# Kernel optimization log

Hardware: AMD Instinct MI355X
Metric: run time of the kernel (lower is better)

Reference implementation:

```python
import jax, jax.numpy as jnp
import numpy as np

ATT_DIM, HID_DIM, EMB_DIM = 512, 1024, 1024
SEQ_LEN, BATCH = 2048, 32


def setup_inputs() -> dict:
    key = jax.random.key(0)
    k1, k2, k3, k4, k5, k6, k7 = jax.random.split(key, 7)
    s_h = 1.0 / np.sqrt(HID_DIM)
    s_e = 1.0 / np.sqrt(EMB_DIM)
    return {
        "hid": jax.random.normal(k1, (BATCH, HID_DIM), dtype=jnp.float32),
        "emb": jax.random.normal(k2, (SEQ_LEN, BATCH, EMB_DIM), dtype=jnp.float32),
        "W_hid": jax.random.uniform(k3, (HID_DIM, ATT_DIM), jnp.float32, -s_h, s_h),
        "b_hid": jax.random.uniform(k4, (ATT_DIM,), jnp.float32, -s_h, s_h),
        "W_emb": jax.random.uniform(k5, (EMB_DIM, ATT_DIM), jnp.float32, -s_e, s_e),
        "b_emb": jax.random.uniform(k6, (ATT_DIM,), jnp.float32, -s_e, s_e),
        "att_v": jax.random.normal(k7, (ATT_DIM,), dtype=jnp.float32),
    }


def reference(hid, emb, W_hid, b_hid, W_emb, b_emb, att_v):
    # hid:  (B, H)   emb: (S, B, E)
    hid_att = hid @ W_hid + b_hid                       # (B, A)
    emb_att = jnp.einsum('sbe,ea->sba', emb, W_emb) + b_emb  # (S, B, A)
    att = jnp.tanh(emb_att + hid_att[None, :, :])       # (S, B, A)
    scores = jnp.einsum('sba,a->bs', att, att_v)        # (B, S)
    weights = jax.nn.softmax(scores, axis=-1)           # (B, S)
    context = jnp.einsum('bs,sbe->be', weights, emb)    # (B, E)
    return context, weights
```

## Files before the change

kernel.cpp:

```cpp
#include <hip/hip_runtime.h>
#include <hip/hip_bf16.h>

#define S_LEN 2048
#define NB    32
#define EMB   1024
#define ATT   512
#define HID   1024

typedef float f32x4  __attribute__((ext_vector_type(4)));
typedef short s16x4  __attribute__((ext_vector_type(4)));
typedef short s16x8  __attribute__((ext_vector_type(8)));

static __device__ __forceinline__ short f2bf(float f) {
    return __builtin_bit_cast(short, __float2bfloat16(f));
}
static __device__ __forceinline__ float bf2f(unsigned short u) {
    unsigned int x = ((unsigned int)u) << 16;
    return __builtin_bit_cast(float, x);
}
static __device__ __forceinline__ float tanh_fast(float x) {
    float e = __expf(2.0f * x);
    return 1.0f - 2.0f / (e + 1.0f);
}

#define GLOAD_LDS16(gp, lp)                                                   \
    __builtin_amdgcn_global_load_lds(                                         \
        (const __attribute__((address_space(1))) void*)(gp),                  \
        (__attribute__((address_space(3))) void*)(uintptr_t)(lp), 16, 0, 0)

__global__ void k_pre(const float* __restrict__ emb,
                      const float* __restrict__ hid,
                      const float* __restrict__ W_hid,
                      const float* __restrict__ b_hid,
                      const float* __restrict__ W_emb,
                      const float* __restrict__ b_emb,
                      unsigned short* __restrict__ embB,
                      float* __restrict__ hid_comb,
                      unsigned short* __restrict__ WT) {
    __shared__ __align__(16) char lds[32768];
    int blk = blockIdx.x, tid = threadIdx.x;
    if (blk >= 576) {
        int cb = blk - 576;
        size_t base = (size_t)cb * 32768;
#pragma unroll
        for (int j = 0; j < 4; ++j)
            GLOAD_LDS16(emb + base + (j * 256 + tid) * 4, lds + (j * 256 + tid) * 16);
        for (int i = 0; i < 8; ++i) {
            int cn = (i + 1) & 7, bn = (i + 1) & 1;
#pragma unroll
            for (int j = 0; j < 4; ++j)
                GLOAD_LDS16(emb + base + cn * 4096 + (j * 256 + tid) * 4,
                            lds + bn * 16384 + (j * 256 + tid) * 16);
            asm volatile("s_waitcnt vmcnt(4)\n\ts_barrier" ::: "memory");
            const char* buf = lds + (i & 1) * 16384;
#pragma unroll
            for (int k = 0; k < 4; ++k) {
                f32x4 x = *(const f32x4*)(buf + k * 4096 + tid * 16);
                s16x4 r;
                r[0] = f2bf(x[0]); r[1] = f2bf(x[1]);
                r[2] = f2bf(x[2]); r[3] = f2bf(x[3]);
                *(s16x4*)(embB + base + i * 4096 + k * 1024 + tid * 4) = r;
            }
            asm volatile("s_waitcnt lgkmcnt(0)\n\ts_barrier" ::: "memory");
        }
    } else if (blk < 64) {
        f32x4 (*red)[64] = (f32x4(*)[64])lds;
        int b    = blk >> 1;
        int a4   = (tid & 63) * 4 + (blk & 1) * 256;
        int ks   = tid >> 6;
        int k0   = ks * 256;
        const float* hr = hid + b * HID + k0;
        const float* wp = W_hid + (size_t)k0 * ATT + a4;
        f32x4 acc = {0.f, 0.f, 0.f, 0.f};
        for (int kb = 0; kb < 256; kb += 8) {
            f32x4 x[8];
#pragma unroll
            for (int u = 0; u < 8; ++u)
                x[u] = *(const f32x4*)(wp + (size_t)(kb + u) * ATT);
            float h[8];
#pragma unroll
            for (int u = 0; u < 8; ++u) h[u] = hr[kb + u];
#pragma unroll
            for (int u = 0; u < 8; ++u) acc += h[u] * x[u];
        }
        red[ks][tid & 63] = acc;
        __syncthreads();
        if (ks == 0) {
            int al = tid & 63;
            f32x4 s = acc + red[1][al] + red[2][al] + red[3][al];
            f32x4 bh = *(const f32x4*)(b_hid + a4);
            f32x4 be = *(const f32x4*)(b_emb + a4);
            *(f32x4*)(hid_comb + b * ATT + a4) = s + bh + be;
        }
    } else {
        float (*tile)[33] = (float(*)[33])lds;
        int b2 = blk - 64;
        int k0 = (b2 & 31) * 32, a0 = (b2 >> 5) * 32;
        int tx = tid & 31, ty = tid >> 5;
#pragma unroll
        for (int i = 0; i < 32; i += 8)
            tile[ty + i][tx] = W_emb[(size_t)(k0 + ty + i) * ATT + a0 + tx];
        __syncthreads();
#pragma unroll
        for (int i = 0; i < 32; i += 8)
            WT[(size_t)(a0 + ty + i) * HID + k0 + tx] =
                (unsigned short)f2bf(tile[tx][ty + i]);
    }
}

__global__ __launch_bounds__(512) void k_gemm_scores(
        const unsigned short* __restrict__ embB,
        const unsigned short* __restrict__ WT,
        const float* __restrict__ hid_comb,
        const float* __restrict__ att_v,
        float* __restrict__ part) {
    __shared__ __align__(16) unsigned short ldsbuf[65536];
    char* L = (char*)ldsbuf;

    int bid = blockIdx.x;
    int t2  = (bid & 7) * 64 + (bid >> 3);
    int mt  = t2 >> 1, nt = t2 & 1;
    int m0  = mt * 256, n0 = nt * 256;

    int tid  = threadIdx.x;
    int lane = tid & 63, wv = tid >> 6;
    int wm = wv >> 2, wn = wv & 3;
    int row_l = lane & 15, kg = lane >> 4;

    int row0 = tid >> 3, pos0 = tid & 7;
    int dst0 = tid * 16, dst1 = tid * 16 + 8192;
    const unsigned short* aG[2][2];
    const unsigned short* bG[2][2];
#pragma unroll
    for (int h = 0; h < 2; ++h) {
        aG[h][0] = embB + (size_t)(m0 + h * 128 + row0) * EMB + ((pos0 ^ (row0 & 7)) * 8);
        aG[h][1] = embB + (size_t)(m0 + h * 128 + row0 + 64) * EMB + ((pos0 ^ (row0 & 7)) * 8);
        bG[h][0] = WT   + (size_t)(n0 + h * 128 + row0) * HID + ((pos0 ^ (row0 & 7)) * 8);
        bG[h][1] = WT   + (size_t)(n0 + h * 128 + row0 + 64) * HID + ((pos0 ^ (row0 & 7)) * 8);
    }

    int aoff[8], boff[4], cx[2];
#pragma unroll
    for (int mf = 0; mf < 8; ++mf)
        aoff[mf] = wm * 16384 + (mf * 16 + row_l) * 128;
#pragma unroll
    for (int nf = 0; nf < 4; ++nf)
        boff[nf] = 65536 + (wn >> 1) * 16384 + (((wn & 1) * 64 + nf * 16 + row_l)) * 128;
#pragma unroll
    for (int ks = 0; ks < 2; ++ks)
        cx[ks] = ((ks * 4 + kg) ^ (row_l & 7)) * 16;

    f32x4 acc[8][4] = {};

#define STAGE_A(H, KT, BUF)                                                    \
    GLOAD_LDS16(aG[H][0] + (KT), L + (BUF) * 32768 + (H) * 16384 + dst0);      \
    GLOAD_LDS16(aG[H][1] + (KT), L + (BUF) * 32768 + (H) * 16384 + dst1);
#define STAGE_B(H, KT, BUF)                                                    \
    GLOAD_LDS16(bG[H][0] + (KT), L + 65536 + (BUF) * 32768 + (H) * 16384 + dst0); \
    GLOAD_LDS16(bG[H][1] + (KT), L + 65536 + (BUF) * 32768 + (H) * 16384 + dst1);

#define QUAD(MB, NBASE, AF, BF)                                                \
    _Pragma("unroll")                                                          \
    for (int ml = 0; ml < 4; ++ml)                                             \
        _Pragma("unroll")                                                      \
        for (int nl = 0; nl < 2; ++nl)                                         \
            _Pragma("unroll")                                                  \
            for (int ks = 0; ks < 2; ++ks)                                     \
                acc[(MB) + ml][(NBASE) + nl] =                                 \
                    __builtin_amdgcn_mfma_f32_16x16x32_bf16(                   \
                        AF[ml][ks], BF[nl][ks], acc[(MB) + ml][(NBASE) + nl],  \
                        0, 0, 0);

    STAGE_A(0, 0, 0) STAGE_A(1, 0, 0) STAGE_B(0, 0, 0) STAGE_B(1, 0, 0)

    for (int t = 0; t < 16; ++t) {
        int bt = t & 1, bn = bt ^ 1;
        int btA = bt * 32768;
        int ktn = ((t + 1) & 15) * 64;
        s16x8 af[4][2], af2[4][2], bfA[2][2], bfB[2][2];

        STAGE_A(0, ktn, bn)
        asm volatile("s_waitcnt vmcnt(2)" ::: "memory");
        asm volatile("s_barrier" ::: "memory");
#pragma unroll
        for (int ml = 0; ml < 4; ++ml)
#pragma unroll
            for (int ks = 0; ks < 2; ++ks)
                af[ml][ks] = *(const s16x8*)(L + btA + aoff[ml] + cx[ks]);
#pragma unroll
        for (int nl = 0; nl < 2; ++nl)
#pragma unroll
            for (int ks = 0; ks < 2; ++ks)
                bfA[nl][ks] = *(const s16x8*)(L + btA + boff[nl] + cx[ks]);
        asm volatile("s_waitcnt lgkmcnt(0)" ::: "memory");
        __builtin_amdgcn_sched_barrier(0);
        __builtin_amdgcn_s_setprio(1);
        QUAD(0, 0, af, bfA)
        __builtin_amdgcn_s_setprio(0);
        asm volatile("s_barrier" ::: "memory");

        STAGE_A(1, ktn, bn)
#pragma unroll
        for (int nl = 0; nl < 2; ++nl)
#pragma unroll
            for (int ks = 0; ks < 2; ++ks)
                bfB[nl][ks] = *(const s16x8*)(L + btA + boff[2 + nl] + cx[ks]);
        asm volatile("s_waitcnt lgkmcnt(0)" ::: "memory");
        __builtin_amdgcn_sched_barrier(0);
        __builtin_amdgcn_s_setprio(1);
        QUAD(0, 2, af, bfB)
        __builtin_amdgcn_s_setprio(0);
        asm volatile("s_barrier" ::: "memory");

        STAGE_B(0, ktn, bn)
#pragma unroll
        for (int ml = 0; ml < 4; ++ml)
#pragma unroll
            for (int ks = 0; ks < 2; ++ks)
                af2[ml][ks] = *(const s16x8*)(L + btA + aoff[4 + ml] + cx[ks]);
        asm volatile("s_waitcnt lgkmcnt(0)" ::: "memory");
        __builtin_amdgcn_sched_barrier(0);
        __builtin_amdgcn_s_setprio(1);
        QUAD(4, 2, af2, bfB)
        __builtin_amdgcn_s_setprio(0);
        asm volatile("s_barrier" ::: "memory");

        STAGE_B(1, ktn, bn)
        __builtin_amdgcn_s_setprio(1);
        QUAD(4, 0, af2, bfA)
        __builtin_amdgcn_s_setprio(0);
        asm volatile("s_barrier" ::: "memory");
    }
#undef STAGE_A
#undef STAGE_B
#undef QUAD

    float vvv[4];
#pragma unroll
    for (int nf = 0; nf < 4; ++nf)
        vvv[nf] = att_v[n0 + wn * 64 + nf * 16 + row_l];

    int slice = nt * 4 + wn;
#pragma unroll
    for (int mf = 0; mf < 8; ++mf) {
#pragma unroll
        for (int j = 0; j < 4; ++j) {
            int m = m0 + wm * 128 + mf * 16 + kg * 4 + j;
            int b = m & 31;
            int s = m >> 5;
            const float* ad = hid_comb + b * ATT + n0 + wn * 64;
            float sum = 0.f;
#pragma unroll
            for (int nf = 0; nf < 4; ++nf) {
                float xv = acc[mf][nf][j] + ad[nf * 16 + row_l];
                sum += tanh_fast(xv) * vvv[nf];
            }
#pragma unroll
            for (int d = 1; d < 16; d <<= 1)
                sum += __shfl_xor(sum, d, 64);
            if (row_l == 0)
                part[slice * (NB * S_LEN) + b * S_LEN + s] = sum;
        }
    }
}

__global__ void k_ctx1s(const unsigned short* __restrict__ embB,
                        const float* __restrict__ part,
                        float* __restrict__ weights,
                        float* __restrict__ cpart) {
    int sc = blockIdx.x, b = blockIdx.y, t = threadIdx.x;
    __shared__ float sm[4], ss[4], wl[128];

    float v[8];
    float mx = -1e30f;
#pragma unroll
    for (int i = 0; i < 8; ++i) {
        int s = i * 256 + t;
        float x = 0.f;
#pragma unroll
        for (int p = 0; p < 8; ++p)
            x += part[p * (NB * S_LEN) + b * S_LEN + s];
        v[i] = x;
        mx = fmaxf(mx, x);
    }
#pragma unroll
    for (int d = 1; d < 64; d <<= 1) mx = fmaxf(mx, __shfl_xor(mx, d, 64));
    if ((t & 63) == 0) sm[t >> 6] = mx;
    __syncthreads();
    mx = fmaxf(fmaxf(sm[0], sm[1]), fmaxf(sm[2], sm[3]));
    float sum = 0.f;
#pragma unroll
    for (int i = 0; i < 8; ++i) {
        v[i] = __expf(v[i] - mx);
        sum += v[i];
    }
#pragma unroll
    for (int d = 1; d < 64; d <<= 1) sum += __shfl_xor(sum, d, 64);
    if ((t & 63) == 0) ss[t >> 6] = sum;
    __syncthreads();
    sum = ss[0] + ss[1] + ss[2] + ss[3];
    float inv = 1.0f / sum;

    if ((t >> 7) == (sc & 1)) wl[t & 127] = v[sc >> 1] * inv;
    if (sc == 0) {
#pragma unroll
        for (int i = 0; i < 8; ++i)
            weights[b * S_LEN + i * 256 + t] = v[i] * inv;
    }
    __syncthreads();

    int par = t >> 7;
    int e0 = (t & 127) * 8;
    float acc[8] = {};
    for (int i = 0; i < 128; i += 2) {
        int s = sc * 128 + i + par;
        float w = wl[i + par];
        s16x8 x = *(const s16x8*)(embB + (((size_t)(s * NB + b)) << 10) + e0);
#pragma unroll
        for (int u = 0; u < 8; ++u)
            acc[u] += w * bf2f((unsigned short)x[u]);
    }
    float* dst = cpart + ((size_t)(sc * 2 + par) * NB + b) * EMB + e0;
    f32x4 lo = {acc[0], acc[1], acc[2], acc[3]};
    f32x4 hi = {acc[4], acc[5], acc[6], acc[7]};
    *(f32x4*)(dst)     = lo;
    *(f32x4*)(dst + 4) = hi;
}

__global__ void k_ctx2(const float* __restrict__ cpart, float* __restrict__ ctx) {
    int i = blockIdx.x * 256 + threadIdx.x;
    float s = 0.f;
#pragma unroll
    for (int p = 0; p < 32; ++p) s += cpart[(size_t)p * (NB * EMB) + i];
    ctx[i] = s;
}

extern "C" void kernel_launch(void* const* d_in, const int* in_sizes, int n_in,
                              void* d_out, int out_size, void* d_ws, size_t ws_size,
                              hipStream_t stream) {
    const float* hid   = (const float*)d_in[0];
    const float* emb   = (const float*)d_in[1];
    const float* W_hid = (const float*)d_in[2];
    const float* b_hid = (const float*)d_in[3];
    const float* W_emb = (const float*)d_in[4];
    const float* b_emb = (const float*)d_in[5];
    const float* att_v = (const float*)d_in[6];

    float* out     = (float*)d_out;
    float* ctx     = out;
    float* weights = out + NB * EMB;

    char* ws = (char*)d_ws;
    float*          part     = (float*)(ws);
    float*          hid_comb = (float*)(ws + 2097152);
    unsigned short* WT       = (unsigned short*)(ws + 2162688);
    unsigned short* embB     = (unsigned short*)(ws + 3211264);
    float*          cpart    = (float*)(ws + 137428992);

    k_pre<<<2624, 256, 0, stream>>>(emb, hid, W_hid, b_hid, W_emb, b_emb,
                                    embB, hid_comb, WT);
    k_gemm_scores<<<512, 512, 0, stream>>>(embB, WT, hid_comb, att_v, part);
    k_ctx1s<<<dim3(16, NB), 256, 0, stream>>>(embB, part, weights, cpart);
    k_ctx2<<<128, 256, 0, stream>>>(cpart, ctx);
}
```

Baseline: 220.8 us.

## Fuse fp32-to-bf16 conversion of emb into GEMM A-tile loading

```diff
diff --git a/kernel.cpp b/kernel.cpp
--- a/kernel.cpp
+++ b/kernel.cpp
@@ -14,10 +14,6 @@
 static __device__ __forceinline__ short f2bf(float f) {
     return __builtin_bit_cast(short, __float2bfloat16(f));
 }
-static __device__ __forceinline__ float bf2f(unsigned short u) {
-    unsigned int x = ((unsigned int)u) << 16;
-    return __builtin_bit_cast(float, x);
-}
 static __device__ __forceinline__ float tanh_fast(float x) {
     float e = __expf(2.0f * x);
     return 1.0f - 2.0f / (e + 1.0f);
@@ -28,42 +24,18 @@
         (const __attribute__((address_space(1))) void*)(gp),                  \
         (__attribute__((address_space(3))) void*)(uintptr_t)(lp), 16, 0, 0)
 
-__global__ void k_pre(const float* __restrict__ emb,
-                      const float* __restrict__ hid,
-                      const float* __restrict__ W_hid,
-                      const float* __restrict__ b_hid,
-                      const float* __restrict__ W_emb,
-                      const float* __restrict__ b_emb,
-                      unsigned short* __restrict__ embB,
-                      float* __restrict__ hid_comb,
-                      unsigned short* __restrict__ WT) {
-    __shared__ __align__(16) char lds[32768];
+#define ORDER_FENCE() asm volatile("" ::: "memory")
+
+__global__ void k_hw(const float* __restrict__ hid,
+                     const float* __restrict__ W_hid,
+                     const float* __restrict__ b_hid,
+                     const float* __restrict__ W_emb,
+                     const float* __restrict__ b_emb,
+                     float* __restrict__ hid_comb,
+                     unsigned short* __restrict__ WT) {
+    __shared__ __align__(16) char lds[8192];
     int blk = blockIdx.x, tid = threadIdx.x;
-    if (blk >= 576) {
-        int cb = blk - 576;
-        size_t base = (size_t)cb * 32768;
-#pragma unroll
-        for (int j = 0; j < 4; ++j)
-            GLOAD_LDS16(emb + base + (j * 256 + tid) * 4, lds + (j * 256 + tid) * 16);
-        for (int i = 0; i < 8; ++i) {
-            int cn = (i + 1) & 7, bn = (i + 1) & 1;
-#pragma unroll
-            for (int j = 0; j < 4; ++j)
-                GLOAD_LDS16(emb + base + cn * 4096 + (j * 256 + tid) * 4,
-                            lds + bn * 16384 + (j * 256 + tid) * 16);
-            asm volatile("s_waitcnt vmcnt(4)\n\ts_barrier" ::: "memory");
-            const char* buf = lds + (i & 1) * 16384;
-#pragma unroll
-            for (int k = 0; k < 4; ++k) {
-                f32x4 x = *(const f32x4*)(buf + k * 4096 + tid * 16);
-                s16x4 r;
-                r[0] = f2bf(x[0]); r[1] = f2bf(x[1]);
-                r[2] = f2bf(x[2]); r[3] = f2bf(x[3]);
-                *(s16x4*)(embB + base + i * 4096 + k * 1024 + tid * 4) = r;
-            }
-            asm volatile("s_waitcnt lgkmcnt(0)\n\ts_barrier" ::: "memory");
-        }
-    } else if (blk < 64) {
+    if (blk < 64) {
         f32x4 (*red)[64] = (f32x4(*)[64])lds;
         int b    = blk >> 1;
         int a4   = (tid & 63) * 4 + (blk & 1) * 256;
@@ -109,7 +81,7 @@
 }
 
 __global__ __launch_bounds__(512) void k_gemm_scores(
-        const unsigned short* __restrict__ embB,
+        const float* __restrict__ emb,
         const unsigned short* __restrict__ WT,
         const float* __restrict__ hid_comb,
         const float* __restrict__ att_v,
@@ -127,16 +99,20 @@
     int wm = wv >> 2, wn = wv & 3;
     int row_l = lane & 15, kg = lane >> 4;
 
+    int ar = tid >> 3, ap = tid & 7;
+    const float* aG0 = emb + (size_t)(m0 + ar) * EMB + ap * 8;
+    const float* aG1 = emb + (size_t)(m0 + 128 + ar) * EMB + ap * 8;
+    int axor = (ap ^ (ar & 7)) * 16;
+    int da0 = ar * 128 + axor;
+    int da1 = (ar + 64) * 128 + axor;
+
     int row0 = tid >> 3, pos0 = tid & 7;
     int dst0 = tid * 16, dst1 = tid * 16 + 8192;
-    const unsigned short* aG[2][2];
     const unsigned short* bG[2][2];
 #pragma unroll
     for (int h = 0; h < 2; ++h) {
-        aG[h][0] = embB + (size_t)(m0 + h * 128 + row0) * EMB + ((pos0 ^ (row0 & 7)) * 8);
-        aG[h][1] = embB + (size_t)(m0 + h * 128 + row0 + 64) * EMB + ((pos0 ^ (row0 & 7)) * 8);
-        bG[h][0] = WT   + (size_t)(n0 + h * 128 + row0) * HID + ((pos0 ^ (row0 & 7)) * 8);
-        bG[h][1] = WT   + (size_t)(n0 + h * 128 + row0 + 64) * HID + ((pos0 ^ (row0 & 7)) * 8);
+        bG[h][0] = WT + (size_t)(n0 + h * 128 + row0) * HID + ((pos0 ^ (row0 & 7)) * 8);
+        bG[h][1] = WT + (size_t)(n0 + h * 128 + row0 + 64) * HID + ((pos0 ^ (row0 & 7)) * 8);
     }
 
     int aoff[8], boff[4], cx[2];
@@ -151,10 +127,29 @@
         cx[ks] = ((ks * 4 + kg) ^ (row_l & 7)) * 16;
 
     f32x4 acc[8][4] = {};
-
-#define STAGE_A(H, KT, BUF)                                                    \
-    GLOAD_LDS16(aG[H][0] + (KT), L + (BUF) * 32768 + (H) * 16384 + dst0);      \
-    GLOAD_LDS16(aG[H][1] + (KT), L + (BUF) * 32768 + (H) * 16384 + dst1);
+    f32x4 Rh0[4], Rh1[4];
+
+#define LOAD_RH(RH, SRC, KT)                                                   \
+    RH[0] = *(const f32x4*)((SRC) + (KT));                                     \
+    RH[1] = *(const f32x4*)((SRC) + (KT) + 4);                                 \
+    RH[2] = *(const f32x4*)((SRC) + (KT) + 64 * EMB);                          \
+    RH[3] = *(const f32x4*)((SRC) + (KT) + 64 * EMB + 4);
+
+#define CVT_WRITE_A(RH, OFF)                                                   \
+    {                                                                          \
+        s16x8 v0, v1;                                                          \
+        v0[0] = f2bf(RH[0][0]); v0[1] = f2bf(RH[0][1]);                        \
+        v0[2] = f2bf(RH[0][2]); v0[3] = f2bf(RH[0][3]);                        \
+        v0[4] = f2bf(RH[1][0]); v0[5] = f2bf(RH[1][1]);                        \
+        v0[6] = f2bf(RH[1][2]); v0[7] = f2bf(RH[1][3]);                        \
+        v1[0] = f2bf(RH[2][0]); v1[1] = f2bf(RH[2][1]);                        \
+        v1[2] = f2bf(RH[2][2]); v1[3] = f2bf(RH[2][3]);                        \
+        v1[4] = f2bf(RH[3][0]); v1[5] = f2bf(RH[3][1]);                        \
+        v1[6] = f2bf(RH[3][2]); v1[7] = f2bf(RH[3][3]);                        \
+        *(s16x8*)(L + (OFF) + da0) = v0;                                       \
+        *(s16x8*)(L + (OFF) + da1) = v1;                                       \
+    }
+
 #define STAGE_B(H, KT, BUF)                                                    \
     GLOAD_LDS16(bG[H][0] + (KT), L + 65536 + (BUF) * 32768 + (H) * 16384 + dst0); \
     GLOAD_LDS16(bG[H][1] + (KT), L + 65536 + (BUF) * 32768 + (H) * 16384 + dst1);
@@ -171,16 +166,25 @@
                         AF[ml][ks], BF[nl][ks], acc[(MB) + ml][(NBASE) + nl],  \
                         0, 0, 0);
 
-    STAGE_A(0, 0, 0) STAGE_A(1, 0, 0) STAGE_B(0, 0, 0) STAGE_B(1, 0, 0)
+    STAGE_B(0, 0, 0) STAGE_B(1, 0, 0)
+    ORDER_FENCE();
+    LOAD_RH(Rh0, aG0, 0) LOAD_RH(Rh1, aG1, 0)
+    asm volatile("s_waitcnt vmcnt(0)" ::: "memory");
+    CVT_WRITE_A(Rh0, 0)
+    CVT_WRITE_A(Rh1, 16384)
+    ORDER_FENCE();
+    LOAD_RH(Rh0, aG0, 64) LOAD_RH(Rh1, aG1, 64)
+    asm volatile("s_waitcnt lgkmcnt(0)\n\ts_barrier" ::: "memory");
 
     for (int t = 0; t < 16; ++t) {
         int bt = t & 1, bn = bt ^ 1;
         int btA = bt * 32768;
         int ktn = ((t + 1) & 15) * 64;
+        int kta = ((t + 2) & 15) * 64;
         s16x8 af[4][2], af2[4][2], bfA[2][2], bfB[2][2];
 
-        STAGE_A(0, ktn, bn)
-        asm volatile("s_waitcnt vmcnt(2)" ::: "memory");
+        STAGE_B(0, ktn, bn)
+        asm volatile("s_waitcnt vmcnt(10)" ::: "memory");
         asm volatile("s_barrier" ::: "memory");
 #pragma unroll
         for (int ml = 0; ml < 4; ++ml)
@@ -199,7 +203,7 @@
         __builtin_amdgcn_s_setprio(0);
         asm volatile("s_barrier" ::: "memory");
 
-        STAGE_A(1, ktn, bn)
+        STAGE_B(1, ktn, bn)
 #pragma unroll
         for (int nl = 0; nl < 2; ++nl)
 #pragma unroll
@@ -212,7 +216,11 @@
         __builtin_amdgcn_s_setprio(0);
         asm volatile("s_barrier" ::: "memory");
 
-        STAGE_B(0, ktn, bn)
+        asm volatile("s_waitcnt vmcnt(8)" ::: "memory");
+        CVT_WRITE_A(Rh0, bn * 32768)
+        ORDER_FENCE();
+        LOAD_RH(Rh0, aG0, kta)
+        ORDER_FENCE();
 #pragma unroll
         for (int ml = 0; ml < 4; ++ml)
 #pragma unroll
@@ -225,13 +233,18 @@
         __builtin_amdgcn_s_setprio(0);
         asm volatile("s_barrier" ::: "memory");
 
-        STAGE_B(1, ktn, bn)
+        asm volatile("s_waitcnt vmcnt(8)" ::: "memory");
+        CVT_WRITE_A(Rh1, bn * 32768 + 16384)
+        ORDER_FENCE();
+        LOAD_RH(Rh1, aG1, kta)
+        ORDER_FENCE();
         __builtin_amdgcn_s_setprio(1);
         QUAD(4, 0, af2, bfA)
         __builtin_amdgcn_s_setprio(0);
-        asm volatile("s_barrier" ::: "memory");
-    }
-#undef STAGE_A
+        asm volatile("s_waitcnt lgkmcnt(0)\n\ts_barrier" ::: "memory");
+    }
+#undef LOAD_RH
+#undef CVT_WRITE_A
 #undef STAGE_B
 #undef QUAD
 
@@ -264,7 +277,7 @@
     }
 }
 
-__global__ void k_ctx1s(const unsigned short* __restrict__ embB,
+__global__ void k_ctx1s(const float* __restrict__ emb,
                         const float* __restrict__ part,
                         float* __restrict__ weights,
                         float* __restrict__ cpart) {
@@ -315,10 +328,13 @@
     for (int i = 0; i < 128; i += 2) {
         int s = sc * 128 + i + par;
         float w = wl[i + par];
-        s16x8 x = *(const s16x8*)(embB + (((size_t)(s * NB + b)) << 10) + e0);
-#pragma unroll
-        for (int u = 0; u < 8; ++u)
-            acc[u] += w * bf2f((unsigned short)x[u]);
+        const float* ep = emb + (((size_t)(s * NB + b)) << 10) + e0;
+        f32x4 x0 = *(const f32x4*)ep;
+        f32x4 x1 = *(const f32x4*)(ep + 4);
+        acc[0] += w * x0[0]; acc[1] += w * x0[1];
+        acc[2] += w * x0[2]; acc[3] += w * x0[3];
+        acc[4] += w * x1[0]; acc[5] += w * x1[1];
+        acc[6] += w * x1[2]; acc[7] += w * x1[3];
     }
     float* dst = cpart + ((size_t)(sc * 2 + par) * NB + b) * EMB + e0;
     f32x4 lo = {acc[0], acc[1], acc[2], acc[3]};
@@ -354,12 +370,10 @@
     float*          part     = (float*)(ws);
     float*          hid_comb = (float*)(ws + 2097152);
     unsigned short* WT       = (unsigned short*)(ws + 2162688);
-    unsigned short* embB     = (unsigned short*)(ws + 3211264);
-    float*          cpart    = (float*)(ws + 137428992);
-
-    k_pre<<<2624, 256, 0, stream>>>(emb, hid, W_hid, b_hid, W_emb, b_emb,
-                                    embB, hid_comb, WT);
-    k_gemm_scores<<<512, 512, 0, stream>>>(embB, WT, hid_comb, att_v, part);
-    k_ctx1s<<<dim3(16, NB), 256, 0, stream>>>(embB, part, weights, cpart);
+    float*          cpart    = (float*)(ws + 3211264);
+
+    k_hw<<<576, 256, 0, stream>>>(hid, W_hid, b_hid, W_emb, b_emb, hid_comb, WT);
+    k_gemm_scores<<<512, 512, 0, stream>>>(emb, WT, hid_comb, att_v, part);
+    k_ctx1s<<<dim3(16, NB), 256, 0, stream>>>(emb, part, weights, cpart);
     k_ctx2<<<128, 256, 0, stream>>>(cpart, ctx);
 }
```

Measured after the change: 197.2 us (median of 2 runs). 10.7% less time.
